# Kernel tuning notes

Hardware: AMD Instinct MI355X
Metric: run time of the kernel (lower is better)

The kernel has to match this reference:

```python
import jax, jax.numpy as jnp
import numpy as np

B, S, C, P, E = 8, 16, 32, 64, 768       # batch, max_spans, max_cand, max_prop, emb_dim
M = S * C                                 # bags per batch = 512
L = M * P                                 # triplet ids per batch = 32768
T = 100000                                # triplet vocab size
NE = 1000000                              # num_entities


def setup_inputs() -> dict:
    key = jax.random.key(0)
    k0, k1, k2, k3, k4, k5 = jax.random.split(key, 6)
    span_embs = jax.random.normal(k0, (B, S, E), dtype=jnp.float32)
    triplet_ids_tr = jax.random.randint(k1, (B, L), 0, T, dtype=jnp.int32)
    # uniform bags: bag i covers [i*P, (i+1)*P); offsets must start at 0 (EmbeddingBag)
    offsets_tr = jnp.tile(jnp.arange(M, dtype=jnp.int32) * P, (B, 1))
    attention_tr = jax.random.uniform(k2, (B, L), dtype=jnp.float32)
    qid_inds = jax.random.randint(k3, (B, M), 0, NE + 1, dtype=jnp.int32)
    emb_weight = jax.random.normal(k4, (T, E), dtype=jnp.float32) * 0.02
    span_W = jax.random.normal(k5, (E, 1), dtype=jnp.float32) * 0.02
    span_b = jnp.zeros((1,), dtype=jnp.float32)
    return {"span_embs": span_embs, "triplet_ids_tr": triplet_ids_tr,
            "offsets_tr": offsets_tr, "attention_tr": attention_tr,
            "qid_inds": qid_inds, "emb_weight": emb_weight,
            "span_W": span_W, "span_b": span_b}


def _embedding_bag_sum(ids, offs, w, table):
    # ids,w: [L]; offs: [M] sorted, offs[0]==0 -> sum-pooled bags [M, E]
    pos = jnp.arange(ids.shape[0])
    seg = jnp.searchsorted(offs, pos, side='right') - 1  # bag id per element
    gathered = table[ids] * w[:, None]                    # [L, E]
    return jax.ops.segment_sum(gathered, seg, num_segments=M)


def reference(span_embs, triplet_ids_tr, offsets_tr, attention_tr, qid_inds,
              emb_weight, span_W, span_b):
    span_scores = span_embs @ span_W + span_b              # [B, S, 1]
    # torch repeat(1, max_cand, 1): whole span block tiled C times along dim 1
    exp_emb = jnp.tile(span_embs, (1, C, 1))               # [B, C*S, E]
    kb_embs = jax.vmap(_embedding_bag_sum, in_axes=(0, 0, 0, None))(
        triplet_ids_tr, offsets_tr, attention_tr, emb_weight)  # [B, M, E]
    mult1 = (kb_embs * exp_emb).reshape(B, S, C, E)
    sum1 = jnp.sum(mult1, axis=3)                          # [B, S, C]
    sm1 = jax.nn.softmax(sum1, axis=1)                     # softmax over spans
    mult2 = (span_scores * sm1).reshape(B, S * C)
    cand_scores = jax.nn.softmax(mult2, axis=1)            # [B, M]
    # one-hot matmul == scatter-add of cand scores onto entity ids
    scatter = jax.vmap(lambda q, s: jnp.zeros(NE + 1, dtype=s.dtype).at[q].add(s))(
        qid_inds, cand_scores)                             # [B, NE+1]
    x0 = scatter[:, :-1, None]                             # drop padding entity -> [B, NE, 1]
    return jax.nn.softmax(x0, axis=1)
```

## Files before the change

### kernel.cpp

```cpp
#include <hip/hip_runtime.h>

#define B   8
#define S   16
#define C   32
#define P   64
#define E   768
#define M   512
#define LL  32768
#define NE  1000000
#define TR  100000

typedef __attribute__((ext_vector_type(8))) short short8;
typedef __attribute__((ext_vector_type(4))) float f32x4;

__device__ __forceinline__ short f2bf(float x) {
    unsigned u = __float_as_uint(x);
    u += 0x7FFFu + ((u >> 16) & 1u);
    return (short)(u >> 16);
}

__device__ __forceinline__ short8 pack8(float4 lo, float4 hi) {
    short8 r;
    r[0] = f2bf(lo.x); r[1] = f2bf(lo.y); r[2] = f2bf(lo.z); r[3] = f2bf(lo.w);
    r[4] = f2bf(hi.x); r[5] = f2bf(hi.y); r[6] = f2bf(hi.z); r[7] = f2bf(hi.w);
    return r;
}

__global__ __launch_bounds__(256) void k_pre_spanbf(
    const float* __restrict__ span, short* __restrict__ spanbf)
{
    const int i = blockIdx.x * 256 + threadIdx.x;
    if (i < B * S * E) spanbf[i] = f2bf(span[i]);
}

__global__ __launch_bounds__(256) void k0_dot_table(
    const float* __restrict__ emb,
    const short* __restrict__ spanbf,
    float*       __restrict__ dt)
{
    const int wave = threadIdx.x >> 6;
    const int lane = threadIdx.x & 63;
    const int mrow = lane & 15;
    const int kq   = lane >> 4;
    const int rbase = blockIdx.x * 128 + wave * 32;

    const int r0 = rbase + mrow;
    const int r1 = r0 + 16;
    const float* a0p = emb + (size_t)(r0 < TR ? r0 : 0) * E;
    const float* a1p = emb + (size_t)(r1 < TR ? r1 : 0) * E;

    f32x4 acc[2][8];
    #pragma unroll
    for (int i = 0; i < 2; ++i)
        #pragma unroll
        for (int j = 0; j < 8; ++j)
            acc[i][j] = f32x4{0.f, 0.f, 0.f, 0.f};

    for (int k0 = 0; k0 < E; k0 += 32) {
        const int koff = k0 + kq * 8;
        const float4 a0lo = *(const float4*)(a0p + koff);
        const float4 a0hi = *(const float4*)(a0p + koff + 4);
        const float4 a1lo = *(const float4*)(a1p + koff);
        const float4 a1hi = *(const float4*)(a1p + koff + 4);
        const short8 A0 = pack8(a0lo, a0hi);
        const short8 A1 = pack8(a1lo, a1hi);
        #pragma unroll
        for (int ct = 0; ct < 8; ++ct) {
            const short8 Bf = *(const short8*)(spanbf + (size_t)(ct * 16 + mrow) * E + koff);
            acc[0][ct] = __builtin_amdgcn_mfma_f32_16x16x32_bf16(A0, Bf, acc[0][ct], 0, 0, 0);
            acc[1][ct] = __builtin_amdgcn_mfma_f32_16x16x32_bf16(A1, Bf, acc[1][ct], 0, 0, 0);
        }
    }

    #pragma unroll
    for (int rt = 0; rt < 2; ++rt) {
        const int orow = rbase + rt * 16 + kq * 4;
        #pragma unroll
        for (int r = 0; r < 4; ++r) {
            if (orow + r < TR) {
                float* o = dt + (size_t)(orow + r) * 128 + mrow;
                #pragma unroll
                for (int ct = 0; ct < 8; ++ct) o[ct * 16] = acc[rt][ct][r];
            }
        }
    }
}

__global__ __launch_bounds__(256) void k1_bagdot(
    const float* __restrict__ dt,
    const int*   __restrict__ ids,
    const float* __restrict__ att,
    float*       __restrict__ sum1)
{
    const int seg  = blockIdx.x * 4 + (threadIdx.x >> 6);
    const int lane = threadIdx.x & 63;
    const int b = seg >> 9;
    const int m = seg & 511;
    const int n = (b << 4) | (m & 15);

    const size_t base = (size_t)b * LL + (size_t)m * P;
    const int   id = ids[base + lane];
    const float a  = att[base + lane];
    float v = a * dt[(size_t)id * 128 + n];

    #pragma unroll
    for (int off = 32; off > 0; off >>= 1)
        v += __shfl_down(v, off, 64);
    if (lane == 0) sum1[seg] = v;
}

__global__ __launch_bounds__(512) void k2_fused(
    const float* __restrict__ sum1,
    const float* __restrict__ span,
    const float* __restrict__ spanW,
    const float* __restrict__ spanb,
    const int*   __restrict__ qids,
    float*       __restrict__ sval,
    float*       __restrict__ invden)
{
    const int b = blockIdx.x;
    const int t = threadIdx.x;

    __shared__ float ls[512];
    __shared__ float cs[512];
    __shared__ int   qs[512];
    __shared__ float ss[16];
    __shared__ float inv_s;

    {
        const int s = t >> 5, j = t & 31;
        const float* sp = span + (size_t)(b * S + s) * E;
        float partial = 0.f;
        for (int e = j; e < E; e += 32) partial = fmaf(sp[e], spanW[e], partial);
        #pragma unroll
        for (int off = 16; off > 0; off >>= 1) partial += __shfl_down(partial, off, 32);
        if (j == 0) ss[s] = partial + spanb[0];
    }

    const float v = sum1[b * M + t];
    ls[t] = v;
    qs[t] = qids[b * M + t];
    __syncthreads();

    const int c = t & 31;
    float mx = -1e30f;
    #pragma unroll
    for (int s2 = 0; s2 < S; ++s2) mx = fmaxf(mx, ls[s2 * 32 + c]);
    float den = 0.f;
    #pragma unroll
    for (int s2 = 0; s2 < S; ++s2) den += expf(ls[s2 * 32 + c] - mx);
    const float m2 = ss[t >> 5] * (expf(v - mx) / den);
    __syncthreads();

    ls[t] = m2; __syncthreads();
    for (int off = 256; off > 0; off >>= 1) {
        if (t < off) ls[t] = fmaxf(ls[t], ls[t + off]);
        __syncthreads();
    }
    const float bigM = ls[0];
    __syncthreads();
    const float ex = expf(m2 - bigM);
    ls[t] = ex; __syncthreads();
    for (int off = 256; off > 0; off >>= 1) {
        if (t < off) ls[t] += ls[t + off];
        __syncthreads();
    }
    const float cand = ex / ls[0];
    __syncthreads();

    cs[t] = cand; __syncthreads();

    const int myq = qs[t];
    float dsum = 0.f;
    int first = 512;
    #pragma unroll 8
    for (int j = 0; j < 512; ++j) {
        const bool match = (qs[j] == myq);
        dsum += match ? cs[j] : 0.f;
        if (match && j < first) first = j;
    }
    const bool owner = (first == t) && (myq < NE);
    const float ev = owner ? expf(dsum) : 1.f;

    ls[t] = owner ? (ev - 1.f) : 0.f;
    __syncthreads();
    for (int off = 256; off > 0; off >>= 1) {
        if (t < off) ls[t] += ls[t + off];
        __syncthreads();
    }
    if (t == 0) {
        const float iv = 1.f / (1.0e6f + ls[0]);
        invden[b] = iv;
        inv_s = iv;
    }
    __syncthreads();

    sval[b * M + t] = owner ? ev * inv_s : 0.f;
}

__global__ __launch_bounds__(256) void k3_fill(
    float* __restrict__ out, const float* __restrict__ invden)
{
    const int i = blockIdx.x * 256 + threadIdx.x;
    if (i >= (B * NE) / 4) return;
    const float v = invden[i / (NE / 4)];
    reinterpret_cast<float4*>(out)[i] = make_float4(v, v, v, v);
}

__global__ __launch_bounds__(512) void k4_scatter(
    const float* __restrict__ sval, const int* __restrict__ qids,
    float* __restrict__ out)
{
    const int b = blockIdx.x, t = threadIdx.x;
    const float v = sval[b * M + t];
    const int   q = qids[b * M + t];
    if (v > 0.f && q < NE) out[(size_t)b * NE + q] = v;
}

extern "C" void kernel_launch(void* const* d_in, const int* in_sizes, int n_in,
                              void* d_out, int out_size, void* d_ws, size_t ws_size,
                              hipStream_t stream)
{
    (void)in_sizes; (void)n_in; (void)out_size; (void)ws_size;

    const float* span_embs = (const float*)d_in[0];
    const int*   ids       = (const int*)  d_in[1];
    const float* att       = (const float*)d_in[3];
    const int*   qids      = (const int*)  d_in[4];
    const float* emb       = (const float*)d_in[5];
    const float* spanW     = (const float*)d_in[6];
    const float* spanb     = (const float*)d_in[7];

    float* out = (float*)d_out;

    float* dt     = (float*)d_ws;
    float* sum1   = dt + (size_t)TR * 128;
    float* sval   = sum1 + B * M;
    float* invden = sval + B * M;
    short* spanbf = (short*)(invden + 64);

    k_pre_spanbf<<<(B * S * E + 255) / 256, 256, 0, stream>>>(span_embs, spanbf);
    k0_dot_table<<<(TR + 127) / 128, 256, 0, stream>>>(emb, spanbf, dt);
    k1_bagdot<<<(B * M) / 4, 256, 0, stream>>>(dt, ids, att, sum1);
    k2_fused<<<B, 512, 0, stream>>>(sum1, span_embs, spanW, spanb, qids, sval, invden);
    k3_fill<<<((B * NE / 4) + 255) / 256, 256, 0, stream>>>(out, invden);
    k4_scatter<<<B, 512, 0, stream>>>(sval, qids, out);
}
```

Before: 597.7 us.

## Stage table rows through double-buffered LDS and pre-swizzle span MFMA fragments

```diff
diff --git a/kernel.cpp b/kernel.cpp
--- a/kernel.cpp
+++ b/kernel.cpp
@@ -9,6 +9,7 @@
 #define LL  32768
 #define NE  1000000
 #define TR  100000
+#define KI  24
 
 typedef __attribute__((ext_vector_type(8))) short short8;
 typedef __attribute__((ext_vector_type(4))) float f32x4;
@@ -26,28 +27,40 @@
     return r;
 }
 
-__global__ __launch_bounds__(256) void k_pre_spanbf(
-    const float* __restrict__ span, short* __restrict__ spanbf)
-{
-    const int i = blockIdx.x * 256 + threadIdx.x;
-    if (i < B * S * E) spanbf[i] = f2bf(span[i]);
-}
-
-__global__ __launch_bounds__(256) void k0_dot_table(
+__global__ __launch_bounds__(256) void k_pre_bfrag(
+    const float* __restrict__ span, short8* __restrict__ bfrag)
+{
+    const int idx = blockIdx.x * 256 + threadIdx.x;
+    if (idx >= KI * 8 * 64) return;
+    const int lane = idx & 63;
+    const int ct   = (idx >> 6) & 7;
+    const int kk   = idx >> 9;
+    const int n = ct * 16 + (lane & 15);
+    const int k = kk * 32 + (lane >> 4) * 8;
+    const float* sp = span + (size_t)n * E + k;
+    const float4 lo = *(const float4*)sp;
+    const float4 hi = *(const float4*)(sp + 4);
+    bfrag[idx] = pack8(lo, hi);
+}
+
+__global__ __launch_bounds__(256, 3) void k0_dot_table(
     const float* __restrict__ emb,
-    const short* __restrict__ spanbf,
+    const short8* __restrict__ bfrag,
     float*       __restrict__ dt)
 {
-    const int wave = threadIdx.x >> 6;
-    const int lane = threadIdx.x & 63;
+    const int tid  = threadIdx.x;
+    const int wave = tid >> 6;
+    const int lane = tid & 63;
     const int mrow = lane & 15;
     const int kq   = lane >> 4;
-    const int rbase = blockIdx.x * 128 + wave * 32;
-
-    const int r0 = rbase + mrow;
-    const int r1 = r0 + 16;
-    const float* a0p = emb + (size_t)(r0 < TR ? r0 : 0) * E;
-    const float* a1p = emb + (size_t)(r1 < TR ? r1 : 0) * E;
+    const int rbase = blockIdx.x * 128;
+
+    __shared__ short8 Abuf[2][8][64];
+
+    const int srow  = tid >> 3;
+    const int kpart = tid & 7;
+    const int dlane = (kpart >> 1) * 16;
+    const int dsub  = (kpart & 1) * 4;
 
     f32x4 acc[2][8];
     #pragma unroll
@@ -56,25 +69,58 @@
         for (int j = 0; j < 8; ++j)
             acc[i][j] = f32x4{0.f, 0.f, 0.f, 0.f};
 
-    for (int k0 = 0; k0 < E; k0 += 32) {
-        const int koff = k0 + kq * 8;
-        const float4 a0lo = *(const float4*)(a0p + koff);
-        const float4 a0hi = *(const float4*)(a0p + koff + 4);
-        const float4 a1lo = *(const float4*)(a1p + koff);
-        const float4 a1hi = *(const float4*)(a1p + koff + 4);
-        const short8 A0 = pack8(a0lo, a0hi);
-        const short8 A1 = pack8(a1lo, a1hi);
+    #pragma unroll
+    for (int p = 0; p < 4; ++p) {
+        const int row  = p * 32 + srow;
+        int grow = rbase + row; if (grow >= TR) grow = TR - 1;
+        const float4 v = *(const float4*)(emb + (size_t)grow * E + kpart * 4);
+        short* dst = (short*)&Abuf[0][row >> 4][dlane + (row & 15)] + dsub;
+        dst[0] = f2bf(v.x); dst[1] = f2bf(v.y); dst[2] = f2bf(v.z); dst[3] = f2bf(v.w);
+    }
+    __syncthreads();
+
+    for (int kk = 0; kk < KI; ++kk) {
+        const int buf = kk & 1;
+
+        const short8 A0 = Abuf[buf][wave * 2][lane];
+        const short8 A1 = Abuf[buf][wave * 2 + 1][lane];
+
+        short8 Bf[8];
+        #pragma unroll
+        for (int ct = 0; ct < 8; ++ct)
+            Bf[ct] = bfrag[(kk * 8 + ct) * 64 + lane];
+
+        float4 nv[4];
+        if (kk + 1 < KI) {
+            #pragma unroll
+            for (int p = 0; p < 4; ++p) {
+                const int row = p * 32 + srow;
+                int grow = rbase + row; if (grow >= TR) grow = TR - 1;
+                nv[p] = *(const float4*)(emb + (size_t)grow * E + (kk + 1) * 32 + kpart * 4);
+            }
+        }
+
         #pragma unroll
         for (int ct = 0; ct < 8; ++ct) {
-            const short8 Bf = *(const short8*)(spanbf + (size_t)(ct * 16 + mrow) * E + koff);
-            acc[0][ct] = __builtin_amdgcn_mfma_f32_16x16x32_bf16(A0, Bf, acc[0][ct], 0, 0, 0);
-            acc[1][ct] = __builtin_amdgcn_mfma_f32_16x16x32_bf16(A1, Bf, acc[1][ct], 0, 0, 0);
-        }
+            acc[0][ct] = __builtin_amdgcn_mfma_f32_16x16x32_bf16(A0, Bf[ct], acc[0][ct], 0, 0, 0);
+            acc[1][ct] = __builtin_amdgcn_mfma_f32_16x16x32_bf16(A1, Bf[ct], acc[1][ct], 0, 0, 0);
+        }
+
+        if (kk + 1 < KI) {
+            #pragma unroll
+            for (int p = 0; p < 4; ++p) {
+                const int row = p * 32 + srow;
+                short* dst = (short*)&Abuf[buf ^ 1][row >> 4][dlane + (row & 15)] + dsub;
+                dst[0] = f2bf(nv[p].x); dst[1] = f2bf(nv[p].y);
+                dst[2] = f2bf(nv[p].z); dst[3] = f2bf(nv[p].w);
+            }
+        }
+        __syncthreads();
     }
 
     #pragma unroll
     for (int rt = 0; rt < 2; ++rt) {
-        const int orow = rbase + rt * 16 + kq * 4;
+        const int orow = rbase + (wave * 2 + rt) * 16 + kq * 4;
         #pragma unroll
         for (int r = 0; r < 4; ++r) {
             if (orow + r < TR) {
@@ -233,14 +279,14 @@
 
     float* out = (float*)d_out;
 
-    float* dt     = (float*)d_ws;
-    float* sum1   = dt + (size_t)TR * 128;
-    float* sval   = sum1 + B * M;
-    float* invden = sval + B * M;
-    short* spanbf = (short*)(invden + 64);
-
-    k_pre_spanbf<<<(B * S * E + 255) / 256, 256, 0, stream>>>(span_embs, spanbf);
-    k0_dot_table<<<(TR + 127) / 128, 256, 0, stream>>>(emb, spanbf, dt);
+    float*  dt     = (float*)d_ws;
+    float*  sum1   = dt + (size_t)TR * 128;
+    float*  sval   = sum1 + B * M;
+    float*  invden = sval + B * M;
+    short8* bfrag  = (short8*)(invden + 64);
+
+    k_pre_bfrag<<<(KI * 8 * 64 + 255) / 256, 256, 0, stream>>>(span_embs, bfrag);
+    k0_dot_table<<<(TR + 127) / 128, 256, 0, stream>>>(emb, bfrag, dt);
     k1_bagdot<<<(B * M) / 4, 256, 0, stream>>>(dt, ids, att, sum1);
     k2_fused<<<B, 512, 0, stream>>>(sum1, span_embs, spanW, spanb, qids, sval, invden);
     k3_fill<<<((B * NE / 4) + 255) / 256, 256, 0, stream>>>(out, invden);
```

Result: faster. 523.8 us (-12.4%).
